# Kernel optimization log

Hardware: AMD Instinct MI355X
Metric: run time of the kernel (lower is better)

Reference implementation:

```python
import jax, jax.numpy as jnp
import numpy as np
import math

B, T, D, H, P, NPASS = 2, 2048, 1024, 16, 256, 3


def setup_inputs() -> dict:
    key = jax.random.key(0)
    ks = jax.random.split(key, 8)
    x = jax.random.normal(ks[0], (B, T, D), jnp.float32)
    scale_gamma = 1.0 + 0.1 * jax.random.normal(ks[1], (D,), jnp.float32)
    scale_beta = 0.1 * jax.random.normal(ks[2], (D,), jnp.float32)
    qkv_w = 0.02 * jax.random.normal(ks[3], (3 * D, D), jnp.float32)
    o_w = 0.02 * jax.random.normal(ks[4], (D, D), jnp.float32)
    norm1_w = jnp.ones((D,), jnp.float32)
    norm2_w = jnp.ones((D,), jnp.float32)
    angles = 0.1 * jax.random.normal(ks[5], (NPASS, P), jnp.float32)
    gate = jnp.ones((NPASS, D), jnp.float32)
    bias = jnp.zeros((NPASS, D), jnp.float32)
    # seeded random permutations matching torch.manual_seed(42+p*1000); torch.randperm
    pis, pjs = [], []
    for p in range(NPASS):
        rng = np.random.RandomState(42 + p * 1000)
        perm = rng.permutation(D)
        pis.append(perm[:P])
        pjs.append(perm[P:2 * P])
    pi = jnp.asarray(np.stack(pis), jnp.int32)
    pj = jnp.asarray(np.stack(pjs), jnp.int32)
    return dict(x=x, scale_gamma=scale_gamma, scale_beta=scale_beta, qkv_w=qkv_w,
                o_w=o_w, norm1_w=norm1_w, norm2_w=norm2_w, angles=angles,
                gate=gate, bias=bias, pi=pi, pj=pj)


def _rmsnorm(x, w):
    eps = jnp.finfo(x.dtype).eps
    return x * jax.lax.rsqrt(jnp.mean(x * x, axis=-1, keepdims=True) + eps) * w


def reference(x, scale_gamma, scale_beta, qkv_w, o_w, norm1_w, norm2_w,
              angles, gate, bias, pi, pj):
    Bs, Ts, Ds = x.shape
    hd = Ds // H
    # --- attention branch ---
    h = _rmsnorm(x, norm1_w) * scale_gamma + scale_beta
    qkv = (h @ qkv_w.T).reshape(Bs, Ts, 3, H, hd)
    qkv = jnp.moveaxis(qkv, 2, 0)            # [3, B, T, H, hd]
    q, k, v = (jnp.swapaxes(qkv[i], 1, 2) for i in range(3))  # [B, H, T, hd]
    scores = jnp.einsum('bhqd,bhkd->bhqk', q, k) / math.sqrt(hd)
    causal = jnp.tril(jnp.ones((Ts, Ts), bool))
    scores = jnp.where(causal, scores, -jnp.inf)
    attn = jax.nn.softmax(scores, axis=-1)
    out = jnp.einsum('bhqk,bhkd->bhqd', attn, v)
    out = jnp.swapaxes(out, 1, 2).reshape(Bs, Ts, Ds)
    x = x + out @ o_w.T
    # --- rotation pseudo-FFN branch ---
    h = _rmsnorm(x, norm2_w) * scale_gamma + scale_beta
    r = h
    for p in range(NPASS):
        cos_a = jnp.cos(angles[p])
        sin_a = jnp.sin(angles[p])
        hi = r[..., pi[p]]
        hj = r[..., pj[p]]
        r = r.at[..., pi[p]].set(hi * cos_a - hj * sin_a)
        r = r.at[..., pj[p]].set(hi * sin_a + hj * cos_a)
        r = jax.nn.silu(r * gate[p] + bias[p])
    return x + r - h
```

## Files before the change

kernel.cpp:

```cpp
#include <hip/hip_runtime.h>
#include <hip/hip_bf16.h>

#define B_ 2
#define T_ 2048
#define D_ 1024
#define H_ 16
#define HD_ 64
#define NP_ 3
#define P_ 256

#define SCALE2 0.18033688011112042f

typedef short bf16x8 __attribute__((ext_vector_type(8)));
typedef float f32x4 __attribute__((ext_vector_type(4)));

__device__ __forceinline__ float bf2f(__hip_bfloat16 v) { return __bfloat162float(v); }
__device__ __forceinline__ __hip_bfloat16 f2bf(float v) { return __float2bfloat16(v); }

__device__ __forceinline__ unsigned pack2bf(float a, float b) {
    union { __hip_bfloat16 h; unsigned short u; } ua, ub;
    ua.h = f2bf(a); ub.h = f2bf(b);
    return (unsigned)ua.u | ((unsigned)ub.u << 16);
}

#define GLOAD_LDS16(gp, lp) \
    __builtin_amdgcn_global_load_lds( \
        (const __attribute__((address_space(1))) void*)(gp), \
        (__attribute__((address_space(3))) void*)(lp), 16, 0, 0)

__global__ __launch_bounds__(256) void detect_kernel(
    const unsigned short* __restrict__ xs, int* __restrict__ flag)
{
    __shared__ int cnt;
    if (threadIdx.x == 0) cnt = 0;
    __syncthreads();
    int bad = 0;
    for (int i = threadIdx.x; i < 16384; i += 256) {
        int e = (xs[i] >> 7) & 0xFF;
        if (e >= 0xB8) bad++;
    }
    if (bad) atomicAdd(&cnt, bad);
    __syncthreads();
    if (threadIdx.x == 0) *flag = (cnt >= 8) ? 1 : 0;
}

__global__ __launch_bounds__(256) void cvt16_2_kernel(
    const void* __restrict__ a, const void* __restrict__ bsrc,
    __hip_bfloat16* __restrict__ da, __hip_bfloat16* __restrict__ db,
    int na, int ntot, const int* __restrict__ flag)
{
    int i = blockIdx.x * 256 + threadIdx.x;
    if (i >= ntot) return;
    int f = *flag;
    if (i < na)
        da[i] = f ? f2bf(((const float*)a)[i]) : ((const __hip_bfloat16*)a)[i];
    else {
        int k = i - na;
        db[k] = f ? f2bf(((const float*)bsrc)[k]) : ((const __hip_bfloat16*)bsrc)[k];
    }
}

__global__ __launch_bounds__(256) void cvt_small_kernel(
    const void* __restrict__ g,  const void* __restrict__ b,
    const void* __restrict__ n1, const void* __restrict__ n2,
    const void* __restrict__ ang, const void* __restrict__ gt,
    const void* __restrict__ bi,
    float* __restrict__ dst, const int* __restrict__ flag)
{
    int i = blockIdx.x * 256 + threadIdx.x;
    if (i >= 11008) return;
    const void* src; int off;
    if      (i < 1024) { src = g;   off = i; }
    else if (i < 2048) { src = b;   off = i - 1024; }
    else if (i < 3072) { src = n1;  off = i - 2048; }
    else if (i < 4096) { src = n2;  off = i - 3072; }
    else if (i < 4864) { src = ang; off = i - 4096; }
    else if (i < 7936) { src = gt;  off = i - 4864; }
    else               { src = bi;  off = i - 7936; }
    dst[i] = (*flag) ? ((const float*)src)[off]
                     : bf2f(((const __hip_bfloat16*)src)[off]);
}

__global__ __launch_bounds__(256) void rmsnorm1_kernel(
    const void* __restrict__ xraw,
    const float* __restrict__ gamma,
    const float* __restrict__ beta,
    const float* __restrict__ w,
    const int* __restrict__ flag,
    __hip_bfloat16* __restrict__ out)
{
    int row = blockIdx.x;
    int t = threadIdx.x;
    int f = *flag;
    float eps = f ? 1.1920929e-7f : 0.0078125f;
    float v[4];
    if (f) {
        const float4 xv = ((const float4*)((const float*)xraw + (size_t)row * D_))[t];
        v[0] = xv.x; v[1] = xv.y; v[2] = xv.z; v[3] = xv.w;
    } else {
        const __hip_bfloat16* xr = (const __hip_bfloat16*)xraw + (size_t)row * D_;
#pragma unroll
        for (int c = 0; c < 4; c++) v[c] = bf2f(xr[t * 4 + c]);
    }
    float ss = 0.f;
#pragma unroll
    for (int c = 0; c < 4; c++) ss += v[c] * v[c];
#pragma unroll
    for (int m = 32; m; m >>= 1) ss += __shfl_xor(ss, m, 64);
    __shared__ float red[4];
    int wv = t >> 6;
    if ((t & 63) == 0) red[wv] = ss;
    __syncthreads();
    float scale = rsqrtf((red[0] + red[1] + red[2] + red[3]) * (1.0f / D_) + eps);
#pragma unroll
    for (int c = 0; c < 4; c++) {
        int e = t * 4 + c;
        size_t idx = (size_t)row * D_ + e;
        out[idx] = f2bf(v[c] * scale * w[e] * gamma[e] + beta[e]);
    }
}

__global__ __launch_bounds__(256) void gemm_bt_bf16_kernel(
    const __hip_bfloat16* __restrict__ A,
    const __hip_bfloat16* __restrict__ Bm,
    __hip_bfloat16* __restrict__ C,
    int M, int N, int K, int nscale, float qscale)
{
    __shared__ __attribute__((aligned(16))) __hip_bfloat16 As[128 * 32];
    __shared__ __attribute__((aligned(16))) __hip_bfloat16 Bs[128 * 32];
    int tid = threadIdx.x;
    int bm = blockIdx.y, bn = blockIdx.x;
    int lane = tid & 63, wv = tid >> 6;
    int wm = wv >> 1, wn = wv & 1;
    int q = lane >> 4, mr = lane & 15;

    f32x4 acc[4][4] = {};

    for (int k0 = 0; k0 < K; k0 += 32) {
#pragma unroll
        for (int s = 0; s < 2; s++) {
            int e = (s * 256 + tid) * 8;
            int r = e >> 5, c = e & 31;
            GLOAD_LDS16(&A[(size_t)(bm * 128 + r) * K + k0 + c], &As[e]);
            GLOAD_LDS16(&Bm[(size_t)(bn * 128 + r) * K + k0 + c], &Bs[e]);
        }
        __syncthreads();
        bf16x8 af[4], bfr[4];
#pragma unroll
        for (int i = 0; i < 4; i++)
            af[i] = *(const bf16x8*)(&As[(wm * 64 + i * 16 + mr) * 32 + q * 8]);
#pragma unroll
        for (int j = 0; j < 4; j++)
            bfr[j] = *(const bf16x8*)(&Bs[(wn * 64 + j * 16 + mr) * 32 + q * 8]);
#pragma unroll
        for (int i = 0; i < 4; i++)
#pragma unroll
            for (int j = 0; j < 4; j++)
                acc[i][j] = __builtin_amdgcn_mfma_f32_16x16x32_bf16(af[i], bfr[j], acc[i][j], 0, 0, 0);
        __syncthreads();
    }

#pragma unroll
    for (int i = 0; i < 4; i++)
#pragma unroll
        for (int r = 0; r < 4; r++) {
            int m = bm * 128 + wm * 64 + i * 16 + q * 4 + r;
#pragma unroll
            for (int j = 0; j < 4; j++) {
                int n = bn * 128 + wn * 64 + j * 16 + mr;
                float vv = acc[i][j][r];
                if (n < nscale) vv *= qscale;
                C[(size_t)m * N + n] = f2bf(vv);
            }
        }
}

__global__ __launch_bounds__(256) void gemm_bt_resid_kernel(
    const __hip_bfloat16* __restrict__ A,
    const __hip_bfloat16* __restrict__ Bm,
    const void* __restrict__ xraw,
    const int* __restrict__ flag,
    float* __restrict__ C,
    int M, int N, int K)
{
    __shared__ __attribute__((aligned(16))) __hip_bfloat16 As[128 * 32];
    __shared__ __attribute__((aligned(16))) __hip_bfloat16 Bs[128 * 32];
    int tid = threadIdx.x;
    int bm = blockIdx.y, bn = blockIdx.x;
    int lane = tid & 63, wv = tid >> 6;
    int wm = wv >> 1, wn = wv & 1;
    int q = lane >> 4, mr = lane & 15;
    int f = *flag;

    f32x4 acc[4][4] = {};

    for (int k0 = 0; k0 < K; k0 += 32) {
#pragma unroll
        for (int s = 0; s < 2; s++) {
            int e = (s * 256 + tid) * 8;
            int r = e >> 5, c = e & 31;
            GLOAD_LDS16(&A[(size_t)(bm * 128 + r) * K + k0 + c], &As[e]);
            GLOAD_LDS16(&Bm[(size_t)(bn * 128 + r) * K + k0 + c], &Bs[e]);
        }
        __syncthreads();
        bf16x8 af[4], bfr[4];
#pragma unroll
        for (int i = 0; i < 4; i++)
            af[i] = *(const bf16x8*)(&As[(wm * 64 + i * 16 + mr) * 32 + q * 8]);
#pragma unroll
        for (int j = 0; j < 4; j++)
            bfr[j] = *(const bf16x8*)(&Bs[(wn * 64 + j * 16 + mr) * 32 + q * 8]);
#pragma unroll
        for (int i = 0; i < 4; i++)
#pragma unroll
            for (int j = 0; j < 4; j++)
                acc[i][j] = __builtin_amdgcn_mfma_f32_16x16x32_bf16(af[i], bfr[j], acc[i][j], 0, 0, 0);
        __syncthreads();
    }

#pragma unroll
    for (int i = 0; i < 4; i++)
#pragma unroll
        for (int r = 0; r < 4; r++) {
            int m = bm * 128 + wm * 64 + i * 16 + q * 4 + r;
#pragma unroll
            for (int j = 0; j < 4; j++) {
                int n = bn * 128 + wn * 64 + j * 16 + mr;
                size_t idx = (size_t)m * N + n;
                float rv = f ? ((const float*)xraw)[idx]
                             : bf2f(((const __hip_bfloat16*)xraw)[idx]);
                C[idx] = rv + acc[i][j][r];
            }
        }
}

__global__ __launch_bounds__(256, 4) void attn_kernel(
    const __hip_bfloat16* __restrict__ qkv,
    __hip_bfloat16* __restrict__ attn_out)
{
    __shared__ __attribute__((aligned(16))) __hip_bfloat16 Ks[2][64 * 64];
    __shared__ __attribute__((aligned(16))) __hip_bfloat16 Vts[2][64 * 64];
    __shared__ __attribute__((aligned(16))) unsigned int Pd[4 * 512];

    int id = blockIdx.x;
    int half = (id ^ (id >> 8)) & 1;
    int w4 = (id >> 1) & 15;
    int qt = half ? 31 - w4 : w4;
    int bh = (id >> 5) & 31;
    int b = bh >> 4, h = bh & 15;
    int tid = threadIdx.x, lane = tid & 63, wv = tid >> 6;
    int q = lane >> 4, mr = lane & 15;
    int m8 = mr & 7;

    const size_t rs3 = 3 * D_;
    const __hip_bfloat16* qp = qkv + (size_t)(b * T_) * rs3 + h * HD_;
    const __hip_bfloat16* kp = qp + D_;
    const __hip_bfloat16* vp = qp + 2 * D_;

    int sr = tid >> 2;
    int sc = (tid & 3) * 16;
    int lc0 = sc >> 3;
    int swk = sr & 7;
    int kk_ = (tid & 31) * 2;
    int dd = (tid >> 5) * 8;
    int vlc = kk_ >> 3, voff = kk_ & 7;

    bf16x8 aq0, aq1;
    {
        const __hip_bfloat16* qrow = qp + (size_t)(qt * 64 + wv * 16 + mr) * rs3;
        aq0 = *(const bf16x8*)(qrow + q * 8);
        aq1 = *(const bf16x8*)(qrow + 32 + q * 8);
    }

    bf16x8 kr0 = *(const bf16x8*)(kp + (size_t)sr * rs3 + sc);
    bf16x8 kr1 = *(const bf16x8*)(kp + (size_t)sr * rs3 + sc + 8);
    bf16x8 vr0 = *(const bf16x8*)(vp + (size_t)kk_ * rs3 + dd);
    bf16x8 vr1 = *(const bf16x8*)(vp + (size_t)(kk_ + 1) * rs3 + dd);
    *(bf16x8*)(&Ks[0][sr * 64 + ((lc0 ^ swk) * 8)]) = kr0;
    *(bf16x8*)(&Ks[0][sr * 64 + (((lc0 + 1) ^ swk) * 8)]) = kr1;
    {
        unsigned int* vd = (unsigned int*)&Vts[0][0];
#pragma unroll
        for (int i = 0; i < 8; i++) {
            unsigned int wd = ((unsigned int)(unsigned short)vr0[i]) |
                              (((unsigned int)(unsigned short)vr1[i]) << 16);
            vd[((dd + i) * 64 + ((vlc ^ i) * 8 + voff)) >> 1] = wd;
        }
    }
    __syncthreads();

    float m_run = -INFINITY, l_run = 0.f;
    f32x4 o_acc[4] = {};
    unsigned int* Pw = &Pd[wv * 512];
    int qloc = wv * 16 + mr;

    for (int s = 0; s <= qt; s++) {
        int buf = s & 1;

        if (s < qt) {
            int ktn = s + 1;
            kr0 = *(const bf16x8*)(kp + (size_t)(ktn * 64 + sr) * rs3 + sc);
            kr1 = *(const bf16x8*)(kp + (size_t)(ktn * 64 + sr) * rs3 + sc + 8);
            vr0 = *(const bf16x8*)(vp + (size_t)(ktn * 64 + kk_) * rs3 + dd);
            vr1 = *(const bf16x8*)(vp + (size_t)(ktn * 64 + kk_ + 1) * rs3 + dd);
        }

        f32x4 sv[4] = {};
        {
            const __hip_bfloat16* Kb = &Ks[buf][0];
#pragma unroll
            for (int jn = 0; jn < 4; jn++)
                sv[jn] = __builtin_amdgcn_mfma_f32_16x16x32_bf16(
                    *(const bf16x8*)(&Kb[(jn * 16 + mr) * 64 + ((q ^ m8) * 8)]),
                    aq0, sv[jn], 0, 0, 0);
#pragma unroll
            for (int jn = 0; jn < 4; jn++)
                sv[jn] = __builtin_amdgcn_mfma_f32_16x16x32_bf16(
                    *(const bf16x8*)(&Kb[(jn * 16 + mr) * 64 + (((4 + q) ^ m8) * 8)]),
                    aq1, sv[jn], 0, 0, 0);
        }

        if (s == qt) {
#pragma unroll
            for (int jn = 0; jn < 4; jn++)
#pragma unroll
                for (int r = 0; r < 4; r++)
                    if (jn * 16 + q * 4 + r > qloc) sv[jn][r] = -1e30f;
        }

        float mx = fmaxf(fmaxf(sv[0][0], sv[0][1]), fmaxf(sv[0][2], sv[0][3]));
#pragma unroll
        for (int jn = 1; jn < 4; jn++)
            mx = fmaxf(mx, fmaxf(fmaxf(sv[jn][0], sv[jn][1]), fmaxf(sv[jn][2], sv[jn][3])));
        mx = fmaxf(mx, __shfl_xor(mx, 16, 64));
        mx = fmaxf(mx, __shfl_xor(mx, 32, 64));
        float mn = fmaxf(m_run, mx);
        float alpha = exp2f(m_run - mn);
        m_run = mn;
        float psum = 0.f;
#pragma unroll
        for (int jn = 0; jn < 4; jn++)
#pragma unroll
            for (int r = 0; r < 4; r++) {
                float p = exp2f(sv[jn][r] - mn);
                sv[jn][r] = p;
                psum += p;
            }
        psum += __shfl_xor(psum, 16, 64);
        psum += __shfl_xor(psum, 32, 64);
        l_run = l_run * alpha + psum;
#pragma unroll
        for (int dt = 0; dt < 4; dt++)
#pragma unroll
            for (int r = 0; r < 4; r++)
                o_acc[dt][r] *= alpha;

#pragma unroll
        for (int jn = 0; jn < 4; jn++) {
            uint2 val;
            val.x = pack2bf(sv[jn][0], sv[jn][1]);
            val.y = pack2bf(sv[jn][2], sv[jn][3]);
            int dw4 = 2 * jn + (q >> 1);
            *(uint2*)(&Pw[mr * 32 + ((dw4 ^ m8) << 2) + 2 * (q & 1)]) = val;
        }

#pragma unroll
        for (int kk = 0; kk < 2; kk++) {
            bf16x8 bp = *(const bf16x8*)(&Pw[mr * 32 + (((4 * kk + q) ^ m8) << 2)]);
#pragma unroll
            for (int dt = 0; dt < 4; dt++) {
                bf16x8 bv = *(const bf16x8*)(&Vts[buf][(dt * 16 + mr) * 64 + (((kk * 4 + q) ^ m8) * 8)]);
                o_acc[dt] = __builtin_amdgcn_mfma_f32_16x16x32_bf16(bv, bp, o_acc[dt], 0, 0, 0);
            }
        }

        if (s < qt) {
            *(bf16x8*)(&Ks[buf ^ 1][sr * 64 + ((lc0 ^ swk) * 8)]) = kr0;
            *(bf16x8*)(&Ks[buf ^ 1][sr * 64 + (((lc0 + 1) ^ swk) * 8)]) = kr1;
            unsigned int* vd = (unsigned int*)&Vts[buf ^ 1][0];
#pragma unroll
            for (int i = 0; i < 8; i++) {
                unsigned int wd = ((unsigned int)(unsigned short)vr0[i]) |
                                  (((unsigned int)(unsigned short)vr1[i]) << 16);
                vd[((dd + i) * 64 + ((vlc ^ i) * 8 + voff)) >> 1] = wd;
            }
        }
        __syncthreads();
    }

    {
        float inv = 1.0f / l_run;
        int trow = qt * 64 + wv * 16 + mr;
        __hip_bfloat16* op = attn_out + (size_t)(b * T_ + trow) * D_ + h * HD_;
#pragma unroll
        for (int dt = 0; dt < 4; dt++) {
            uint2 val;
            val.x = pack2bf(o_acc[dt][0] * inv, o_acc[dt][1] * inv);
            val.y = pack2bf(o_acc[dt][2] * inv, o_acc[dt][3] * inv);
            *(uint2*)(op + dt * 16 + q * 4) = val;
        }
    }
}

__global__ __launch_bounds__(256) void final_kernel(
    const float* __restrict__ xn,
    const float* __restrict__ gamma,
    const float* __restrict__ beta,
    const float* __restrict__ w2,
    const float* __restrict__ angles,
    const float* __restrict__ gate,
    const float* __restrict__ bias,
    const int* __restrict__ pi,
    const int* __restrict__ pj,
    const int* __restrict__ flag,
    void* __restrict__ outp)
{
    __shared__ float rbuf[D_];
    __shared__ float red[4];
    int row = blockIdx.x, t = threadIdx.x;
    int f = *flag;
    float eps = f ? 1.1920929e-7f : 0.0078125f;
    const float* xr = xn + (size_t)row * D_;
    float x4[4];
    float ss = 0.f;
#pragma unroll
    for (int c = 0; c < 4; c++) { x4[c] = xr[t * 4 + c]; ss += x4[c] * x4[c]; }
#pragma unroll
    for (int m = 32; m; m >>= 1) ss += __shfl_xor(ss, m, 64);
    int wv = t >> 6;
    if ((t & 63) == 0) red[wv] = ss;
    __syncthreads();
    float scale = rsqrtf((red[0] + red[1] + red[2] + red[3]) * (1.0f / D_) + eps);
    float hloc[4];
#pragma unroll
    for (int c = 0; c < 4; c++) {
        int e = t * 4 + c;
        float hv = x4[c] * scale * w2[e] * gamma[e] + beta[e];
        hloc[c] = hv;
        rbuf[e] = hv;
    }
    __syncthreads();
    for (int p = 0; p < NP_; p++) {
        float a = angles[p * P_ + t];
        float ca = __cosf(a), sa = __sinf(a);
        int ip = pi[p * P_ + t], jp = pj[p * P_ + t];
        float hi = rbuf[ip], hj = rbuf[jp];
        rbuf[ip] = hi * ca - hj * sa;
        rbuf[jp] = hi * sa + hj * ca;
        __syncthreads();
#pragma unroll
        for (int c = 0; c < 4; c++) {
            int e = t * 4 + c;
            float v = rbuf[e] * gate[p * D_ + e] + bias[p * D_ + e];
            rbuf[e] = v / (1.f + __expf(-v));
        }
        __syncthreads();
    }
#pragma unroll
    for (int c = 0; c < 4; c++) {
        int e = t * 4 + c;
        float ov = x4[c] + rbuf[e] - hloc[c];
        size_t idx = (size_t)row * D_ + e;
        if (f) ((float*)outp)[idx] = ov;
        else   ((__hip_bfloat16*)outp)[idx] = f2bf(ov);
    }
}

extern "C" void kernel_launch(void* const* d_in, const int* in_sizes, int n_in,
                              void* d_out, int out_size, void* d_ws, size_t ws_size,
                              hipStream_t stream)
{
    const void* x      = d_in[0];
    const void* gamma  = d_in[1];
    const void* beta   = d_in[2];
    const void* qkv_w  = d_in[3];
    const void* o_w    = d_in[4];
    const void* n1w    = d_in[5];
    const void* n2w    = d_in[6];
    const void* angles = d_in[7];
    const void* gate   = d_in[8];
    const void* bias   = d_in[9];
    const int* pi = (const int*)d_in[10];
    const int* pj = (const int*)d_in[11];

    const int M = B_ * T_;
    char* ws = (char*)d_ws;
    const size_t MB = 1u << 20;
    int*   flag   = (int*)ws;
    float* smalls = (float*)(ws + 4096);
    float* gf   = smalls;
    float* bf   = smalls + 1024;
    float* n1f  = smalls + 2048;
    float* n2f  = smalls + 3072;
    float* angf = smalls + 4096;
    float* gtf  = smalls + 4864;
    float* bif  = smalls + 7936;
    __hip_bfloat16* wbf  = (__hip_bfloat16*)(ws + 17 * MB);
    __hip_bfloat16* owbf = (__hip_bfloat16*)(ws + 23 * MB);
    __hip_bfloat16* h1   = (__hip_bfloat16*)(ws + 25 * MB);
    __hip_bfloat16* qkv  = (__hip_bfloat16*)(ws + 33 * MB);
    float*          xnew = (float*)         (ws + 33 * MB);

    detect_kernel<<<1, 256, 0, stream>>>((const unsigned short*)x, flag);

    cvt_small_kernel<<<43, 256, 0, stream>>>(gamma, beta, n1w, n2w, angles, gate, bias,
                                             smalls, flag);
    cvt16_2_kernel<<<(4 * D_ * D_ + 255) / 256, 256, 0, stream>>>(
        qkv_w, o_w, wbf, owbf, 3 * D_ * D_, 4 * D_ * D_, flag);

    rmsnorm1_kernel<<<M, 256, 0, stream>>>(x, gf, bf, n1f, flag, h1);

    gemm_bt_bf16_kernel<<<dim3(3 * D_ / 128, M / 128), 256, 0, stream>>>(
        h1, wbf, qkv, M, 3 * D_, D_, D_, SCALE2);

    attn_kernel<<<dim3(1024), 256, 0, stream>>>(qkv, h1);

    gemm_bt_resid_kernel<<<dim3(D_ / 128, M / 128), 256, 0, stream>>>(
        h1, owbf, x, flag, xnew, M, D_, D_);

    final_kernel<<<M, 256, 0, stream>>>(xnew, gf, bf, n2f, angf, gtf, bif,
                                        pi, pj, flag, d_out);
}
```

Measured before the change: 255.6 us.

## Process two query tiles per attention block to reuse K/V loads

Each attention block now handles 128 query rows as two 64-row tiles that share the same K/V tiles from shared memory, which halves K/V global loads and LDS staging per query. The grid halves to 512 blocks, tiles are scheduled largest-first, and occupancy hint drops to 3 blocks per CU. In exchange there are more registers and LDS per block, fewer blocks to balance causal work, and the first tile's work is branched off on its extra diagonal step.

```diff
diff --git a/kernel.cpp b/kernel.cpp
--- a/kernel.cpp
+++ b/kernel.cpp
@@ -234,23 +234,22 @@
         }
 }
 
-__global__ __launch_bounds__(256, 4) void attn_kernel(
+__global__ __launch_bounds__(256, 3) void attn_kernel(
     const __hip_bfloat16* __restrict__ qkv,
     __hip_bfloat16* __restrict__ attn_out)
 {
     __shared__ __attribute__((aligned(16))) __hip_bfloat16 Ks[2][64 * 64];
     __shared__ __attribute__((aligned(16))) __hip_bfloat16 Vts[2][64 * 64];
-    __shared__ __attribute__((aligned(16))) unsigned int Pd[4 * 512];
+    __shared__ __attribute__((aligned(16))) unsigned int Pd[4 * 1024];
 
     int id = blockIdx.x;
-    int half = (id ^ (id >> 8)) & 1;
-    int w4 = (id >> 1) & 15;
-    int qt = half ? 31 - w4 : w4;
-    int bh = (id >> 5) & 31;
+    int qt = 15 - (id & 15);
+    int bh = id >> 4;
     int b = bh >> 4, h = bh & 15;
     int tid = threadIdx.x, lane = tid & 63, wv = tid >> 6;
     int q = lane >> 4, mr = lane & 15;
     int m8 = mr & 7;
+    int cnt = 2 * qt + 2;
 
     const size_t rs3 = 3 * D_;
     const __hip_bfloat16* qp = qkv + (size_t)(b * T_) * rs3 + h * HD_;
@@ -265,11 +264,14 @@
     int dd = (tid >> 5) * 8;
     int vlc = kk_ >> 3, voff = kk_ & 7;
 
-    bf16x8 aq0, aq1;
+    bf16x8 aq0, aq1, aq2, aq3;
     {
-        const __hip_bfloat16* qrow = qp + (size_t)(qt * 64 + wv * 16 + mr) * rs3;
-        aq0 = *(const bf16x8*)(qrow + q * 8);
-        aq1 = *(const bf16x8*)(qrow + 32 + q * 8);
+        const __hip_bfloat16* qrow1 = qp + (size_t)(qt * 128 + wv * 16 + mr) * rs3;
+        aq0 = *(const bf16x8*)(qrow1 + q * 8);
+        aq1 = *(const bf16x8*)(qrow1 + 32 + q * 8);
+        const __hip_bfloat16* qrow2 = qrow1 + (size_t)64 * rs3;
+        aq2 = *(const bf16x8*)(qrow2 + q * 8);
+        aq3 = *(const bf16x8*)(qrow2 + 32 + q * 8);
     }
 
     bf16x8 kr0 = *(const bf16x8*)(kp + (size_t)sr * rs3 + sc);
@@ -289,15 +291,17 @@
     }
     __syncthreads();
 
-    float m_run = -INFINITY, l_run = 0.f;
-    f32x4 o_acc[4] = {};
-    unsigned int* Pw = &Pd[wv * 512];
+    float m1 = -INFINITY, l1 = 0.f, m2 = -INFINITY, l2 = 0.f;
+    f32x4 o1[4] = {}, o2[4] = {};
+    unsigned int* Pw1 = &Pd[wv * 1024];
+    unsigned int* Pw2 = Pw1 + 512;
     int qloc = wv * 16 + mr;
 
-    for (int s = 0; s <= qt; s++) {
+    for (int s = 0; s < cnt; s++) {
         int buf = s & 1;
-
-        if (s < qt) {
+        int do1 = (s <= 2 * qt);
+
+        if (s + 1 < cnt) {
             int ktn = s + 1;
             kr0 = *(const bf16x8*)(kp + (size_t)(ktn * 64 + sr) * rs3 + sc);
             kr1 = *(const bf16x8*)(kp + (size_t)(ktn * 64 + sr) * rs3 + sc + 8);
@@ -305,76 +309,134 @@
             vr1 = *(const bf16x8*)(vp + (size_t)(ktn * 64 + kk_ + 1) * rs3 + dd);
         }
 
-        f32x4 sv[4] = {};
+        f32x4 sv1[4] = {}, sv2[4] = {};
         {
             const __hip_bfloat16* Kb = &Ks[buf][0];
 #pragma unroll
+            for (int jn = 0; jn < 4; jn++) {
+                bf16x8 ka = *(const bf16x8*)(&Kb[(jn * 16 + mr) * 64 + ((q ^ m8) * 8)]);
+                bf16x8 kb = *(const bf16x8*)(&Kb[(jn * 16 + mr) * 64 + (((4 + q) ^ m8) * 8)]);
+                sv1[jn] = __builtin_amdgcn_mfma_f32_16x16x32_bf16(ka, aq0, sv1[jn], 0, 0, 0);
+                sv1[jn] = __builtin_amdgcn_mfma_f32_16x16x32_bf16(kb, aq1, sv1[jn], 0, 0, 0);
+                sv2[jn] = __builtin_amdgcn_mfma_f32_16x16x32_bf16(ka, aq2, sv2[jn], 0, 0, 0);
+                sv2[jn] = __builtin_amdgcn_mfma_f32_16x16x32_bf16(kb, aq3, sv2[jn], 0, 0, 0);
+            }
+        }
+
+        if (s == 2 * qt) {
+#pragma unroll
             for (int jn = 0; jn < 4; jn++)
-                sv[jn] = __builtin_amdgcn_mfma_f32_16x16x32_bf16(
-                    *(const bf16x8*)(&Kb[(jn * 16 + mr) * 64 + ((q ^ m8) * 8)]),
-                    aq0, sv[jn], 0, 0, 0);
+#pragma unroll
+                for (int r = 0; r < 4; r++)
+                    if (jn * 16 + q * 4 + r > qloc) sv1[jn][r] = -1e30f;
+        }
+        if (s == cnt - 1) {
 #pragma unroll
             for (int jn = 0; jn < 4; jn++)
-                sv[jn] = __builtin_amdgcn_mfma_f32_16x16x32_bf16(
-                    *(const bf16x8*)(&Kb[(jn * 16 + mr) * 64 + (((4 + q) ^ m8) * 8)]),
-                    aq1, sv[jn], 0, 0, 0);
-        }
-
-        if (s == qt) {
+#pragma unroll
+                for (int r = 0; r < 4; r++)
+                    if (jn * 16 + q * 4 + r > qloc) sv2[jn][r] = -1e30f;
+        }
+
+        if (do1) {
+            float mx = fmaxf(fmaxf(sv1[0][0], sv1[0][1]), fmaxf(sv1[0][2], sv1[0][3]));
+#pragma unroll
+            for (int jn = 1; jn < 4; jn++)
+                mx = fmaxf(mx, fmaxf(fmaxf(sv1[jn][0], sv1[jn][1]), fmaxf(sv1[jn][2], sv1[jn][3])));
+            mx = fmaxf(mx, __shfl_xor(mx, 16, 64));
+            mx = fmaxf(mx, __shfl_xor(mx, 32, 64));
+            float mn = fmaxf(m1, mx);
+            float alpha = exp2f(m1 - mn);
+            m1 = mn;
+            float psum = 0.f;
 #pragma unroll
             for (int jn = 0; jn < 4; jn++)
 #pragma unroll
+                for (int r = 0; r < 4; r++) {
+                    float p = exp2f(sv1[jn][r] - mn);
+                    sv1[jn][r] = p;
+                    psum += p;
+                }
+            psum += __shfl_xor(psum, 16, 64);
+            psum += __shfl_xor(psum, 32, 64);
+            l1 = l1 * alpha + psum;
+#pragma unroll
+            for (int dt = 0; dt < 4; dt++)
+#pragma unroll
                 for (int r = 0; r < 4; r++)
-                    if (jn * 16 + q * 4 + r > qloc) sv[jn][r] = -1e30f;
-        }
-
-        float mx = fmaxf(fmaxf(sv[0][0], sv[0][1]), fmaxf(sv[0][2], sv[0][3]));
-#pragma unroll
-        for (int jn = 1; jn < 4; jn++)
-            mx = fmaxf(mx, fmaxf(fmaxf(sv[jn][0], sv[jn][1]), fmaxf(sv[jn][2], sv[jn][3])));
-        mx = fmaxf(mx, __shfl_xor(mx, 16, 64));
-        mx = fmaxf(mx, __shfl_xor(mx, 32, 64));
-        float mn = fmaxf(m_run, mx);
-        float alpha = exp2f(m_run - mn);
-        m_run = mn;
-        float psum = 0.f;
-#pragma unroll
-        for (int jn = 0; jn < 4; jn++)
-#pragma unroll
-            for (int r = 0; r < 4; r++) {
-                float p = exp2f(sv[jn][r] - mn);
-                sv[jn][r] = p;
-                psum += p;
-            }
-        psum += __shfl_xor(psum, 16, 64);
-        psum += __shfl_xor(psum, 32, 64);
-        l_run = l_run * alpha + psum;
-#pragma unroll
-        for (int dt = 0; dt < 4; dt++)
-#pragma unroll
-            for (int r = 0; r < 4; r++)
-                o_acc[dt][r] *= alpha;
-
-#pragma unroll
-        for (int jn = 0; jn < 4; jn++) {
-            uint2 val;
-            val.x = pack2bf(sv[jn][0], sv[jn][1]);
-            val.y = pack2bf(sv[jn][2], sv[jn][3]);
-            int dw4 = 2 * jn + (q >> 1);
-            *(uint2*)(&Pw[mr * 32 + ((dw4 ^ m8) << 2) + 2 * (q & 1)]) = val;
-        }
-
-#pragma unroll
-        for (int kk = 0; kk < 2; kk++) {
-            bf16x8 bp = *(const bf16x8*)(&Pw[mr * 32 + (((4 * kk + q) ^ m8) << 2)]);
-#pragma unroll
-            for (int dt = 0; dt < 4; dt++) {
-                bf16x8 bv = *(const bf16x8*)(&Vts[buf][(dt * 16 + mr) * 64 + (((kk * 4 + q) ^ m8) * 8)]);
-                o_acc[dt] = __builtin_amdgcn_mfma_f32_16x16x32_bf16(bv, bp, o_acc[dt], 0, 0, 0);
-            }
-        }
-
-        if (s < qt) {
+                    o1[dt][r] *= alpha;
+#pragma unroll
+            for (int jn = 0; jn < 4; jn++) {
+                uint2 val;
+                val.x = pack2bf(sv1[jn][0], sv1[jn][1]);
+                val.y = pack2bf(sv1[jn][2], sv1[jn][3]);
+                int dw4 = 2 * jn + (q >> 1);
+                *(uint2*)(&Pw1[mr * 32 + ((dw4 ^ m8) << 2) + 2 * (q & 1)]) = val;
+            }
+        }
+
+        {
+            float mx = fmaxf(fmaxf(sv2[0][0], sv2[0][1]), fmaxf(sv2[0][2], sv2[0][3]));
+#pragma unroll
+            for (int jn = 1; jn < 4; jn++)
+                mx = fmaxf(mx, fmaxf(fmaxf(sv2[jn][0], sv2[jn][1]), fmaxf(sv2[jn][2], sv2[jn][3])));
+            mx = fmaxf(mx, __shfl_xor(mx, 16, 64));
+            mx = fmaxf(mx, __shfl_xor(mx, 32, 64));
+            float mn = fmaxf(m2, mx);
+            float alpha = exp2f(m2 - mn);
+            m2 = mn;
+            float psum = 0.f;
+#pragma unroll
+            for (int jn = 0; jn < 4; jn++)
+#pragma unroll
+                for (int r = 0; r < 4; r++) {
+                    float p = exp2f(sv2[jn][r] - mn);
+                    sv2[jn][r] = p;
+                    psum += p;
+                }
+            psum += __shfl_xor(psum, 16, 64);
+            psum += __shfl_xor(psum, 32, 64);
+            l2 = l2 * alpha + psum;
+#pragma unroll
+            for (int dt = 0; dt < 4; dt++)
+#pragma unroll
+                for (int r = 0; r < 4; r++)
+                    o2[dt][r] *= alpha;
+#pragma unroll
+            for (int jn = 0; jn < 4; jn++) {
+                uint2 val;
+                val.x = pack2bf(sv2[jn][0], sv2[jn][1]);
+                val.y = pack2bf(sv2[jn][2], sv2[jn][3]);
+                int dw4 = 2 * jn + (q >> 1);
+                *(uint2*)(&Pw2[mr * 32 + ((dw4 ^ m8) << 2) + 2 * (q & 1)]) = val;
+            }
+        }
+
+        if (do1) {
+#pragma unroll
+            for (int kk = 0; kk < 2; kk++) {
+                bf16x8 bp1 = *(const bf16x8*)(&Pw1[mr * 32 + (((4 * kk + q) ^ m8) << 2)]);
+                bf16x8 bp2 = *(const bf16x8*)(&Pw2[mr * 32 + (((4 * kk + q) ^ m8) << 2)]);
+#pragma unroll
+                for (int dt = 0; dt < 4; dt++) {
+                    bf16x8 bv = *(const bf16x8*)(&Vts[buf][(dt * 16 + mr) * 64 + (((kk * 4 + q) ^ m8) * 8)]);
+                    o1[dt] = __builtin_amdgcn_mfma_f32_16x16x32_bf16(bv, bp1, o1[dt], 0, 0, 0);
+                    o2[dt] = __builtin_amdgcn_mfma_f32_16x16x32_bf16(bv, bp2, o2[dt], 0, 0, 0);
+                }
+            }
+        } else {
+#pragma unroll
+            for (int kk = 0; kk < 2; kk++) {
+                bf16x8 bp2 = *(const bf16x8*)(&Pw2[mr * 32 + (((4 * kk + q) ^ m8) << 2)]);
+#pragma unroll
+                for (int dt = 0; dt < 4; dt++) {
+                    bf16x8 bv = *(const bf16x8*)(&Vts[buf][(dt * 16 + mr) * 64 + (((kk * 4 + q) ^ m8) * 8)]);
+                    o2[dt] = __builtin_amdgcn_mfma_f32_16x16x32_bf16(bv, bp2, o2[dt], 0, 0, 0);
+                }
+            }
+        }
+
+        if (s + 1 < cnt) {
             *(bf16x8*)(&Ks[buf ^ 1][sr * 64 + ((lc0 ^ swk) * 8)]) = kr0;
             *(bf16x8*)(&Ks[buf ^ 1][sr * 64 + (((lc0 + 1) ^ swk) * 8)]) = kr1;
             unsigned int* vd = (unsigned int*)&Vts[buf ^ 1][0];
@@ -389,14 +451,26 @@
     }
 
     {
-        float inv = 1.0f / l_run;
-        int trow = qt * 64 + wv * 16 + mr;
+        float inv = 1.0f / l1;
+        int trow = qt * 128 + wv * 16 + mr;
         __hip_bfloat16* op = attn_out + (size_t)(b * T_ + trow) * D_ + h * HD_;
 #pragma unroll
         for (int dt = 0; dt < 4; dt++) {
             uint2 val;
-            val.x = pack2bf(o_acc[dt][0] * inv, o_acc[dt][1] * inv);
-            val.y = pack2bf(o_acc[dt][2] * inv, o_acc[dt][3] * inv);
+            val.x = pack2bf(o1[dt][0] * inv, o1[dt][1] * inv);
+            val.y = pack2bf(o1[dt][2] * inv, o1[dt][3] * inv);
+            *(uint2*)(op + dt * 16 + q * 4) = val;
+        }
+    }
+    {
+        float inv = 1.0f / l2;
+        int trow = qt * 128 + 64 + wv * 16 + mr;
+        __hip_bfloat16* op = attn_out + (size_t)(b * T_ + trow) * D_ + h * HD_;
+#pragma unroll
+        for (int dt = 0; dt < 4; dt++) {
+            uint2 val;
+            val.x = pack2bf(o2[dt][0] * inv, o2[dt][1] * inv);
+            val.y = pack2bf(o2[dt][2] * inv, o2[dt][3] * inv);
             *(uint2*)(op + dt * 16 + q * 4) = val;
         }
     }
@@ -513,7 +587,7 @@
     gemm_bt_bf16_kernel<<<dim3(3 * D_ / 128, M / 128), 256, 0, stream>>>(
         h1, wbf, qkv, M, 3 * D_, D_, D_, SCALE2);
 
-    attn_kernel<<<dim3(1024), 256, 0, stream>>>(qkv, h1);
+    attn_kernel<<<dim3(512), 256, 0, stream>>>(qkv, h1);
 
     gemm_bt_resid_kernel<<<dim3(D_ / 128, M / 128), 256, 0, stream>>>(
         h1, owbf, x, flag, xnew, M, D_, D_);
```

Result: slower. 294.7 us (+15.3%).
